# Optimization experiments

Hardware: AMD Instinct MI355X
Metric: run time of the kernel (lower is better)

Reference implementation:

```python
import jax, jax.numpy as jnp
import numpy as np

E = 384      # dim_embd
H = 6        # n_heads
D = E // H   # head dim = 64
T_MAX = 256  # block_size
EPS = 1e-5


def setup_inputs() -> dict:
    key = jax.random.key(0)
    ks = jax.random.split(key, 12)
    B, T = 128, 256
    s_in = (1.0 / E) ** 0.5
    s_ff = (1.0 / (4 * E)) ** 0.5
    return {
        "x": jax.random.normal(ks[0], (B, T, E), jnp.float32),
        # per-head projections stacked to match torch concat order: [E, H*D]
        "wq": jax.random.normal(ks[1], (E, E), jnp.float32) * s_in,
        "wk": jax.random.normal(ks[2], (E, E), jnp.float32) * s_in,
        "wv": jax.random.normal(ks[3], (E, E), jnp.float32) * s_in,
        "w_proj": jax.random.normal(ks[4], (E, E), jnp.float32) * s_in,
        "b_proj": jnp.zeros((E,), jnp.float32),
        "w1": jax.random.normal(ks[5], (E, 4 * E), jnp.float32) * s_in,
        "b1": jnp.zeros((4 * E,), jnp.float32),
        "w2": jax.random.normal(ks[6], (4 * E, E), jnp.float32) * s_ff,
        "b2": jnp.zeros((E,), jnp.float32),
        "g1": jnp.ones((E,), jnp.float32),
        "beta1": jnp.zeros((E,), jnp.float32),
        "g2": jnp.ones((E,), jnp.float32),
        "beta2": jnp.zeros((E,), jnp.float32),
    }


def _layernorm(x, g, b):
    mu = jnp.mean(x, axis=-1, keepdims=True)
    var = jnp.mean(jnp.square(x - mu), axis=-1, keepdims=True)
    return (x - mu) * jax.lax.rsqrt(var + EPS) * g + b


def _attention(x, wq, wk, wv, w_proj, b_proj):
    B, T, C = x.shape
    # batched per-head projections: [B,T,H,D]
    q = (x @ wq).reshape(B, T, H, D)
    k = (x @ wk).reshape(B, T, H, D)
    v = (x @ wv).reshape(B, T, H, D)
    # NOTE: original scales by C**-0.5 with C = full embed dim (384)
    scale = C ** (-0.5)
    scores = jnp.einsum("bthd,bshd->bhts", q, k) * scale
    mask = jnp.tril(jnp.ones((T, T), bool))
    scores = jnp.where(mask, scores, -jnp.inf)
    wei = jax.nn.softmax(scores, axis=-1)  # dropout = identity (eval)
    out = jnp.einsum("bhts,bshd->bthd", wei, v).reshape(B, T, C)
    return out @ w_proj + b_proj


def reference(x, wq, wk, wv, w_proj, b_proj, w1, b1, w2, b2, g1, beta1, g2, beta2):
    x = x + _attention(_layernorm(x, g1, beta1), wq, wk, wv, w_proj, b_proj)
    h = _layernorm(x, g2, beta2)
    h = jax.nn.relu(h @ w1 + b1) @ w2 + b2  # dropout = identity (eval)
    return x + h
```

## Files before the change

### kernel.cpp

```cpp
#include <hip/hip_runtime.h>
#include <hip/hip_bf16.h>

typedef __attribute__((ext_vector_type(8))) short bf16x8;
typedef __attribute__((ext_vector_type(4))) float f32x4;

#define MFMA_BF16(a, b, c) __builtin_amdgcn_mfma_f32_16x16x32_bf16((a), (b), (c), 0, 0, 0)

#define E_DIM 384
#define T_SEQ 256
#define B_BATCH 128
#define H_HEADS 6
#define D_HEAD 64
#define NROWS (B_BATCH * T_SEQ)
#define FF_DIM (4 * E_DIM)
#define QKV_LD 1152

__device__ __forceinline__ void load_lds16(const __hip_bfloat16* g, __hip_bfloat16* l) {
    __builtin_amdgcn_global_load_lds(
        (const __attribute__((address_space(1))) void*)g,
        (__attribute__((address_space(3))) void*)l, 16, 0, 0);
}

__device__ __forceinline__ float to_f(float x) { return x; }
__device__ __forceinline__ float to_f(__hip_bfloat16 x) { return __bfloat162float(x); }

__global__ void tcast_all_kernel(const float* __restrict__ wq, const float* __restrict__ wk,
                                 const float* __restrict__ wv, const float* __restrict__ wp,
                                 const float* __restrict__ w1, const float* __restrict__ w2,
                                 __hip_bfloat16* __restrict__ wqkvT, __hip_bfloat16* __restrict__ wpT,
                                 __hip_bfloat16* __restrict__ w1T, __hip_bfloat16* __restrict__ w2T) {
    const int WE = E_DIM * E_DIM;
    const int FE = E_DIM * FF_DIM;
    int idx = blockIdx.x * 256 + threadIdx.x;
    if (idx < 3 * WE) {
        int seg = idx / WE, j = idx - seg * WE;
        const float* W = seg == 0 ? wq : (seg == 1 ? wk : wv);
        int k = j / E_DIM, n = j - k * E_DIM;
        wqkvT[(size_t)seg * WE + (size_t)n * E_DIM + k] = __float2bfloat16(W[j]);
    } else if (idx < 4 * WE) {
        int j = idx - 3 * WE;
        int k = j / E_DIM, n = j - k * E_DIM;
        wpT[(size_t)n * E_DIM + k] = __float2bfloat16(wp[j]);
    } else if (idx < 4 * WE + FE) {
        int j = idx - 4 * WE;
        int k = j / FF_DIM, n = j - k * FF_DIM;
        w1T[(size_t)n * E_DIM + k] = __float2bfloat16(w1[j]);
    } else {
        int j = idx - 4 * WE - FE;
        int k = j / E_DIM, n = j - k * E_DIM;
        w2T[(size_t)n * FF_DIM + k] = __float2bfloat16(w2[j]);
    }
}

template <typename TI>
__global__ __launch_bounds__(256) void ln_kernel(const TI* __restrict__ x,
                                                 const float* __restrict__ g,
                                                 const float* __restrict__ bta,
                                                 __hip_bfloat16* __restrict__ out) {
    int row = blockIdx.x * 4 + (threadIdx.x >> 6);
    int lane = threadIdx.x & 63;
    const TI* xr = x + (size_t)row * E_DIM;
    float vals[6];
    float s = 0.f;
#pragma unroll
    for (int i = 0; i < 3; i++) {
        int c = i * 128 + 2 * lane;
        if constexpr (sizeof(TI) == 4) {
            float2 v = *reinterpret_cast<const float2*>(&xr[c]);
            vals[2 * i] = v.x;
            vals[2 * i + 1] = v.y;
        } else {
            ushort2 u = *reinterpret_cast<const ushort2*>(&xr[c]);
            union { unsigned short us; __hip_bfloat16 h; } a, b2;
            a.us = u.x; b2.us = u.y;
            vals[2 * i] = __bfloat162float(a.h);
            vals[2 * i + 1] = __bfloat162float(b2.h);
        }
        s += vals[2 * i] + vals[2 * i + 1];
    }
#pragma unroll
    for (int off = 1; off < 64; off <<= 1) s += __shfl_xor(s, off, 64);
    float mu = s * (1.f / E_DIM);
    float vv = 0.f;
#pragma unroll
    for (int i = 0; i < 6; i++) {
        float d = vals[i] - mu;
        vv += d * d;
    }
#pragma unroll
    for (int off = 1; off < 64; off <<= 1) vv += __shfl_xor(vv, off, 64);
    float rstd = rsqrtf(vv * (1.f / E_DIM) + 1e-5f);
#pragma unroll
    for (int i = 0; i < 3; i++) {
        int c = i * 128 + 2 * lane;
        float2 gv = *reinterpret_cast<const float2*>(&g[c]);
        float2 bv = *reinterpret_cast<const float2*>(&bta[c]);
        union { ushort2 u; struct { __hip_bfloat16 a, b; } h; } o2;
        o2.h.a = __float2bfloat16((vals[2 * i] - mu) * rstd * gv.x + bv.x);
        o2.h.b = __float2bfloat16((vals[2 * i + 1] - mu) * rstd * gv.y + bv.y);
        *reinterpret_cast<ushort2*>(&out[(size_t)row * E_DIM + c]) = o2.u;
    }
}

template <int EPI, int NW>
__global__ __launch_bounds__(NW * 64, NW == 8 ? 4 : 3) void gemm_kernel(
    const __hip_bfloat16* __restrict__ A, const __hip_bfloat16* __restrict__ BT,
    const float* __restrict__ bias, const void* __restrict__ resid,
    void* __restrict__ outp, int M, int N, int K) {
    constexpr int BM = NW * 32;
    constexpr int T = NW * 64;
    constexpr int BUF = (BM + 128) * 32;
    __shared__ __hip_bfloat16 lds[3 * BUF];
    const int t = threadIdx.x;
    const int w = t >> 6, lane = t & 63;
    const int l16 = lane & 15, lhi = lane >> 4;
    const int wm = w >> 1, wn = w & 1;

    const int nwg = gridDim.x;
    const int bid = blockIdx.x;
    const int cpx = nwg >> 3;
    const int swz = (bid & 7) * cpx + (bid >> 3);
    const int nb = N >> 7;
    const int m0 = (swz / nb) * BM;
    const int n0 = (swz % nb) * 128;

    const int ql = (t & 7) ^ ((t >> 3) & 7);
    const int sr = 2 * (t >> 3) + (ql >> 2);
    const int scol = (ql & 3) * 8;
    const __hip_bfloat16* pa0 = A + (size_t)(m0 + sr) * K + scol;
    const __hip_bfloat16* pa1 = pa0 + (size_t)(T / 4) * K;
    const __hip_bfloat16* pb0 = BT + (size_t)(n0 + sr) * K + scol;
    const __hip_bfloat16* pb1 = pb0 + (size_t)(T / 4) * K;
    const int dstA = t * 8;

    int aoff[4], boff[4];
#pragma unroll
    for (int mr = 0; mr < 4; mr++) {
        int R = wm * 64 + mr * 16 + l16;
        int L = R >> 1;
        int q = (((R & 1) << 2) | lhi) ^ (L & 7);
        aoff[mr] = L * 64 + q * 8;
    }
#pragma unroll
    for (int nr = 0; nr < 4; nr++) {
        int R = wn * 64 + nr * 16 + l16;
        int L = R >> 1;
        int q = (((R & 1) << 2) | lhi) ^ (L & 7);
        boff[nr] = BM * 32 + L * 64 + q * 8;
    }

    f32x4 acc[4][4] = {};
    const int nk = K >> 5;

#define STAGE(sbuf)                                                           \
    {                                                                         \
        __hip_bfloat16* sb_ = &lds[(sbuf) * BUF];                             \
        load_lds16(pa0, sb_ + dstA);                                          \
        load_lds16(pa1, sb_ + T * 8 + dstA);                                  \
        load_lds16(pb0, sb_ + BM * 32 + dstA);                                \
        if constexpr (NW == 4) load_lds16(pb1, sb_ + BM * 32 + T * 8 + dstA); \
        pa0 += 32;                                                            \
        pa1 += 32;                                                            \
        pb0 += 32;                                                            \
        if constexpr (NW == 4) pb1 += 32;                                     \
    }

    STAGE(0);
    STAGE(1);
    int rb = 0, sbx = 2;

    for (int kt = 0; kt < nk; kt++) {
        if (kt + 1 < nk) {
            if constexpr (NW == 8) asm volatile("s_waitcnt vmcnt(3)" ::: "memory");
            else                   asm volatile("s_waitcnt vmcnt(4)" ::: "memory");
        } else {
            asm volatile("s_waitcnt vmcnt(0)" ::: "memory");
        }
        __builtin_amdgcn_s_barrier();
        __builtin_amdgcn_sched_barrier(0);
        if (kt + 2 < nk) STAGE(sbx);
        const __hip_bfloat16* base = &lds[rb * BUF];
        bf16x8 af[4], bg[4];
#pragma unroll
        for (int mr = 0; mr < 4; mr++)
            af[mr] = *reinterpret_cast<const bf16x8*>(base + aoff[mr]);
#pragma unroll
        for (int nr = 0; nr < 4; nr++)
            bg[nr] = *reinterpret_cast<const bf16x8*>(base + boff[nr]);
        __builtin_amdgcn_s_setprio(1);
#pragma unroll
        for (int mr = 0; mr < 4; mr++)
#pragma unroll
            for (int nr = 0; nr < 4; nr++)
                acc[mr][nr] = MFMA_BF16(af[mr], bg[nr], acc[mr][nr]);
        __builtin_amdgcn_s_setprio(0);
        rb = rb == 2 ? 0 : rb + 1;
        sbx = sbx == 2 ? 0 : sbx + 1;
    }
#undef STAGE

    __hip_bfloat16* outb = (__hip_bfloat16*)outp;
    float* outf = (float*)outp;
#pragma unroll
    for (int mr = 0; mr < 4; mr++) {
#pragma unroll
        for (int nr = 0; nr < 4; nr++) {
            const int col = n0 + wn * 64 + nr * 16 + l16;
#pragma unroll
            for (int r = 0; r < 4; r++) {
                const int row = m0 + wm * 64 + mr * 16 + lhi * 4 + r;
                const size_t off = (size_t)row * N + col;
                float v = acc[mr][nr][r];
                if (EPI == 0) {
                    outb[off] = __float2bfloat16(v);
                } else if (EPI == 2) {
                    v += bias[col];
                    outb[off] = __float2bfloat16(v > 0.f ? v : 0.f);
                } else if (EPI == 3) {
                    v += bias[col] + ((const float*)resid)[off];
                    outb[off] = __float2bfloat16(v);
                } else {
                    v += bias[col] + to_f(((const __hip_bfloat16*)resid)[off]);
                    outf[off] = v;
                }
            }
        }
    }
}

__global__ __launch_bounds__(256, 2) void attn_kernel(
    const __hip_bfloat16* __restrict__ qkv, __hip_bfloat16* __restrict__ o) {
    __shared__ __hip_bfloat16 Ks[T_SEQ * 64];
    __shared__ __hip_bfloat16 VTs[64 * 256];
    __shared__ __hip_bfloat16 Ps[4 * 2048];

    const int bh = blockIdx.x;
    const int b = bh / H_HEADS, h = bh - b * H_HEADS;
    const int t = threadIdx.x;
    const int w = t >> 6, lane = t & 63;
    const int l16 = lane & 15, lhi = lane >> 4;
    const int l8 = l16 & 7;
    const size_t rbase = (size_t)b * T_SEQ;
    const int qoff = h * D_HEAD, koff = E_DIM + h * D_HEAD, voff = 2 * E_DIM + h * D_HEAD;
    const float qscale = 0.051031036307982884f * 1.4426950408889634f;

#pragma unroll
    for (int i = 0; i < 8; i++) {
        int idx = i * 256 + t;
        int r = idx >> 3;
        int c8 = idx & 7;
        load_lds16(qkv + (rbase + r) * QKV_LD + koff + ((c8 ^ (r & 7)) << 3),
                   &Ks[idx * 8]);
    }
#pragma unroll
    for (int i = 0; i < 8; i++) {
        int idx = i * 256 + t;
        int r = idx >> 3, d0 = (idx & 7) * 8;
        uint4 val = *reinterpret_cast<const uint4*>(qkv + (rbase + r) * QKV_LD + voff + d0);
        const __hip_bfloat16* p8 = reinterpret_cast<const __hip_bfloat16*>(&val);
        int slot = r >> 3, rin = r & 7;
#pragma unroll
        for (int j = 0; j < 8; j++) {
            int d = d0 + j;
            VTs[d * 256 + ((slot ^ (d & 7)) << 3) + rin] = p8[j];
        }
    }
    __syncthreads();

#pragma unroll
    for (int cp = 0; cp < 2; cp++) {
        const int c = cp ? 7 - w : w;
        bf16x8 qf[2][2];
#pragma unroll
        for (int mr = 0; mr < 2; mr++)
#pragma unroll
            for (int kk = 0; kk < 2; kk++)
                qf[mr][kk] = *reinterpret_cast<const bf16x8*>(
                    qkv + (rbase + c * 32 + mr * 16 + l16) * QKV_LD + qoff + kk * 32 + lhi * 8);

        float mstate[2][4], lstate[2][4];
        f32x4 oacc[2][4] = {};
#pragma unroll
        for (int mr = 0; mr < 2; mr++)
#pragma unroll
            for (int r = 0; r < 4; r++) {
                mstate[mr][r] = -1e30f;
                lstate[mr][r] = 0.f;
            }

        const int njt = (c >> 1) + 1;
        for (int jt = 0; jt < njt; jt++) {
            const bool diag = (jt == (c >> 1));
            f32x4 s[2][4] = {};
#pragma unroll
            for (int kk = 0; kk < 2; kk++) {
                bf16x8 kf[4];
#pragma unroll
                for (int nr = 0; nr < 4; nr++) {
                    int R = jt * 64 + nr * 16 + l16;
                    kf[nr] = *reinterpret_cast<const bf16x8*>(
                        &Ks[R * 64 + (((kk << 2) + lhi) ^ l8) * 8]);
                }
#pragma unroll
                for (int mr = 0; mr < 2; mr++)
#pragma unroll
                    for (int nr = 0; nr < 4; nr++)
                        s[mr][nr] = MFMA_BF16(qf[mr][kk], kf[nr], s[mr][nr]);
            }
#pragma unroll
            for (int mr = 0; mr < 2; mr++) {
#pragma unroll
                for (int r = 0; r < 4; r++) {
                    int qrow = c * 32 + mr * 16 + lhi * 4 + r;
                    float pv[4];
                    float mx = -1e30f;
                    if (diag) {
#pragma unroll
                        for (int nr = 0; nr < 4; nr++) {
                            int kcol = jt * 64 + nr * 16 + l16;
                            float val = s[mr][nr][r] * qscale;
                            if (kcol > qrow) val = -1e30f;
                            pv[nr] = val;
                            mx = fmaxf(mx, val);
                        }
                    } else {
#pragma unroll
                        for (int nr = 0; nr < 4; nr++) {
                            float val = s[mr][nr][r] * qscale;
                            pv[nr] = val;
                            mx = fmaxf(mx, val);
                        }
                    }
#pragma unroll
                    for (int off = 1; off < 16; off <<= 1)
                        mx = fmaxf(mx, __shfl_xor(mx, off, 64));
                    float mold = mstate[mr][r];
                    float mnew = fmaxf(mold, mx);
                    float corr = exp2f(mold - mnew);
                    float psum = 0.f;
#pragma unroll
                    for (int nr = 0; nr < 4; nr++) {
                        float p = exp2f(pv[nr] - mnew);
                        pv[nr] = p;
                        psum += p;
                    }
#pragma unroll
                    for (int off = 1; off < 16; off <<= 1)
                        psum += __shfl_xor(psum, off, 64);
                    lstate[mr][r] = lstate[mr][r] * corr + psum;
                    mstate[mr][r] = mnew;
#pragma unroll
                    for (int dr = 0; dr < 4; dr++) oacc[mr][dr][r] *= corr;
                    int pr = mr * 16 + lhi * 4 + r;
#pragma unroll
                    for (int nr = 0; nr < 4; nr++) {
                        int slot = (nr << 1) + (l16 >> 3);
                        Ps[w * 2048 + pr * 64 + ((slot ^ (pr & 7)) << 3) + l8] =
                            __float2bfloat16(pv[nr]);
                    }
                }
            }
#pragma unroll
            for (int kk = 0; kk < 2; kk++) {
                bf16x8 pa[2], vbf[4];
#pragma unroll
                for (int mr = 0; mr < 2; mr++) {
                    int row = mr * 16 + l16;
                    pa[mr] = *reinterpret_cast<const bf16x8*>(
                        &Ps[w * 2048 + row * 64 + (((kk << 2) + lhi) ^ l8) * 8]);
                }
#pragma unroll
                for (int dr = 0; dr < 4; dr++) {
                    int d = dr * 16 + l16;
                    int slot = (jt << 3) + (kk << 2) + lhi;
                    vbf[dr] = *reinterpret_cast<const bf16x8*>(
                        &VTs[d * 256 + ((slot ^ l8) << 3)]);
                }
#pragma unroll
                for (int mr = 0; mr < 2; mr++)
#pragma unroll
                    for (int dr = 0; dr < 4; dr++)
                        oacc[mr][dr] = MFMA_BF16(pa[mr], vbf[dr], oacc[mr][dr]);
            }
        }

#pragma unroll
        for (int mr = 0; mr < 2; mr++) {
#pragma unroll
            for (int r = 0; r < 4; r++) {
                float rl = 1.f / lstate[mr][r];
                int row = c * 32 + mr * 16 + lhi * 4 + r;
#pragma unroll
                for (int dr = 0; dr < 4; dr++)
                    o[(rbase + row) * E_DIM + h * D_HEAD + dr * 16 + l16] =
                        __float2bfloat16(oacc[mr][dr][r] * rl);
            }
        }
    }
}

extern "C" void kernel_launch(void* const* d_in, const int* in_sizes, int n_in,
                              void* d_out, int out_size, void* d_ws, size_t ws_size,
                              hipStream_t stream) {
    const float* x      = (const float*)d_in[0];
    const float* wq     = (const float*)d_in[1];
    const float* wk     = (const float*)d_in[2];
    const float* wv     = (const float*)d_in[3];
    const float* w_proj = (const float*)d_in[4];
    const float* b_proj = (const float*)d_in[5];
    const float* w1     = (const float*)d_in[6];
    const float* b1     = (const float*)d_in[7];
    const float* w2     = (const float*)d_in[8];
    const float* b2     = (const float*)d_in[9];
    const float* g1     = (const float*)d_in[10];
    const float* bt1    = (const float*)d_in[11];
    const float* g2     = (const float*)d_in[12];
    const float* bt2    = (const float*)d_in[13];
    float* out = (float*)d_out;

    char* ws = (char*)d_ws;
    size_t off = 0;
    auto alloc = [&](size_t bytes) {
        void* p = ws + off;
        off += (bytes + 255) & ~(size_t)255;
        return p;
    };
    const size_t wElems = E_DIM * E_DIM;
    const size_t fElems = E_DIM * FF_DIM;
    const size_t actElems = (size_t)NROWS * E_DIM;
    __hip_bfloat16* wqkvT = (__hip_bfloat16*)alloc(3 * wElems * 2);
    __hip_bfloat16* wpT   = (__hip_bfloat16*)alloc(wElems * 2);
    __hip_bfloat16* w1T   = (__hip_bfloat16*)alloc(fElems * 2);
    __hip_bfloat16* w2T   = (__hip_bfloat16*)alloc(fElems * 2);
    __hip_bfloat16* lnb   = (__hip_bfloat16*)alloc(actElems * 2);
    __hip_bfloat16* x2b   = (__hip_bfloat16*)alloc(actElems * 2);
    __hip_bfloat16* qkv   = (__hip_bfloat16*)alloc(3 * actElems * 2);
    __hip_bfloat16* ab    = (__hip_bfloat16*)alloc(actElems * 2);
    __hip_bfloat16* h1    = qkv;

    tcast_all_kernel<<<6912, 256, 0, stream>>>(wq, wk, wv, w_proj, w1, w2,
                                               wqkvT, wpT, w1T, w2T);

    ln_kernel<float><<<NROWS / 4, 256, 0, stream>>>(x, g1, bt1, lnb);

    gemm_kernel<0, 4><<<(NROWS / 128) * (QKV_LD / 128), 256, 0, stream>>>(
        lnb, wqkvT, nullptr, nullptr, qkv, NROWS, QKV_LD, E_DIM);

    attn_kernel<<<B_BATCH * H_HEADS, 256, 0, stream>>>(qkv, ab);

    gemm_kernel<3, 4><<<(NROWS / 128) * (E_DIM / 128), 256, 0, stream>>>(
        ab, wpT, b_proj, x, x2b, NROWS, E_DIM, E_DIM);

    ln_kernel<__hip_bfloat16><<<NROWS / 4, 256, 0, stream>>>(x2b, g2, bt2, lnb);

    gemm_kernel<2, 8><<<(NROWS / 256) * (FF_DIM / 128), 512, 0, stream>>>(
        lnb, w1T, b1, nullptr, h1, NROWS, FF_DIM, E_DIM);

    gemm_kernel<4, 4><<<(NROWS / 128) * (E_DIM / 128), 256, 0, stream>>>(
        h1, w2T, b2, x2b, out, NROWS, E_DIM, FF_DIM);
}
```

Baseline: 248.7 us.

## Add K=384 GEMM kernel keeping full B panel in LDS, A read directly

Adds a GEMM kernel for K=384 that loads an entire 64x384 panel of the transposed weight into swizzled LDS once. Each of 8 waves then streams its 64 rows of A straight from global memory into registers and runs MFMA. This replaces the pipelined LDS double-tiled GEMM for the QKV, output-projection and FF1 GEMMs. The aim is to drop the per-K-step A staging and barriers, at the cost of uncoalesced A loads with no reuse through LDS and A being re-read once per column block.

```diff
diff --git a/kernel.cpp b/kernel.cpp
--- a/kernel.cpp
+++ b/kernel.cpp
@@ -102,6 +102,101 @@
     }
 }
 
+template <int EPI>
+__global__ __launch_bounds__(512) void breg_gemm_kernel(
+    const __hip_bfloat16* __restrict__ A, const __hip_bfloat16* __restrict__ BT,
+    const float* __restrict__ bias, const float* __restrict__ resid,
+    void* __restrict__ outp, int M, int N) {
+    __shared__ __hip_bfloat16 Bs[64 * 384];
+    const int t = threadIdx.x;
+    const int w = t >> 6, lane = t & 63;
+    const int l16 = lane & 15, lhi = lane >> 4;
+
+    const int nwg = gridDim.x;
+    const int bid = blockIdx.x;
+    const int cpx = nwg >> 3;
+    const int swz = (bid & 7) * cpx + (bid >> 3);
+    const int nb = N >> 6;
+    const int m0 = (swz / nb) * 512;
+    const int n0 = (swz % nb) * 64;
+
+#pragma unroll
+    for (int c = 0; c < 6; c++) {
+        int u = c * 512 + t;
+        int r = u / 48;
+        int qp = u - r * 48;
+        int q = (qp & ~7) | ((qp & 7) ^ (r & 7));
+        load_lds16(BT + (size_t)(n0 + r) * 384 + q * 8, &Bs[u * 8]);
+    }
+
+    const __hip_bfloat16* pa[4][2];
+#pragma unroll
+    for (int mr = 0; mr < 4; mr++)
+#pragma unroll
+        for (int kk = 0; kk < 2; kk++)
+            pa[mr][kk] = A + (size_t)(m0 + w * 64 + mr * 16 + l16) * 384 + kk * 32 + lhi * 8;
+
+    int boff[4][2];
+#pragma unroll
+    for (int nr = 0; nr < 4; nr++)
+#pragma unroll
+        for (int kk = 0; kk < 2; kk++) {
+            int r = nr * 16 + l16;
+            boff[nr][kk] = r * 384 + (((kk * 4 + lhi) ^ (r & 7)) << 3);
+        }
+
+    __syncthreads();
+
+    f32x4 acc[4][4] = {};
+#pragma unroll
+    for (int kc = 0; kc < 6; kc++) {
+        bf16x8 af[4][2], bf_[4][2];
+#pragma unroll
+        for (int mr = 0; mr < 4; mr++)
+#pragma unroll
+            for (int kk = 0; kk < 2; kk++) {
+                af[mr][kk] = *reinterpret_cast<const bf16x8*>(pa[mr][kk]);
+                pa[mr][kk] += 64;
+            }
+#pragma unroll
+        for (int nr = 0; nr < 4; nr++)
+#pragma unroll
+            for (int kk = 0; kk < 2; kk++)
+                bf_[nr][kk] = *reinterpret_cast<const bf16x8*>(&Bs[boff[nr][kk] + kc * 64]);
+#pragma unroll
+        for (int kk = 0; kk < 2; kk++)
+#pragma unroll
+            for (int mr = 0; mr < 4; mr++)
+#pragma unroll
+                for (int nr = 0; nr < 4; nr++)
+                    acc[mr][nr] = MFMA_BF16(af[mr][kk], bf_[nr][kk], acc[mr][nr]);
+    }
+
+    __hip_bfloat16* outb = (__hip_bfloat16*)outp;
+#pragma unroll
+    for (int mr = 0; mr < 4; mr++) {
+#pragma unroll
+        for (int nr = 0; nr < 4; nr++) {
+            const int col = n0 + nr * 16 + l16;
+#pragma unroll
+            for (int r = 0; r < 4; r++) {
+                const int row = m0 + w * 64 + mr * 16 + lhi * 4 + r;
+                const size_t off = (size_t)row * N + col;
+                float v = acc[mr][nr][r];
+                if (EPI == 0) {
+                    outb[off] = __float2bfloat16(v);
+                } else if (EPI == 2) {
+                    v += bias[col];
+                    outb[off] = __float2bfloat16(v > 0.f ? v : 0.f);
+                } else {
+                    v += bias[col] + resid[off];
+                    outb[off] = __float2bfloat16(v);
+                }
+            }
+        }
+    }
+}
+
 template <int EPI, int NW>
 __global__ __launch_bounds__(NW * 64, NW == 8 ? 4 : 3) void gemm_kernel(
     const __hip_bfloat16* __restrict__ A, const __hip_bfloat16* __restrict__ BT,
@@ -443,18 +538,18 @@
 
     ln_kernel<float><<<NROWS / 4, 256, 0, stream>>>(x, g1, bt1, lnb);
 
-    gemm_kernel<0, 4><<<(NROWS / 128) * (QKV_LD / 128), 256, 0, stream>>>(
-        lnb, wqkvT, nullptr, nullptr, qkv, NROWS, QKV_LD, E_DIM);
+    breg_gemm_kernel<0><<<(NROWS / 512) * (QKV_LD / 64), 512, 0, stream>>>(
+        lnb, wqkvT, nullptr, nullptr, qkv, NROWS, QKV_LD);
 
     attn_kernel<<<B_BATCH * H_HEADS, 256, 0, stream>>>(qkv, ab);
 
-    gemm_kernel<3, 4><<<(NROWS / 128) * (E_DIM / 128), 256, 0, stream>>>(
-        ab, wpT, b_proj, x, x2b, NROWS, E_DIM, E_DIM);
+    breg_gemm_kernel<3><<<(NROWS / 512) * (E_DIM / 64), 512, 0, stream>>>(
+        ab, wpT, b_proj, x, x2b, NROWS, E_DIM);
 
     ln_kernel<__hip_bfloat16><<<NROWS / 4, 256, 0, stream>>>(x2b, g2, bt2, lnb);
 
-    gemm_kernel<2, 8><<<(NROWS / 256) * (FF_DIM / 128), 512, 0, stream>>>(
-        lnb, w1T, b1, nullptr, h1, NROWS, FF_DIM, E_DIM);
+    breg_gemm_kernel<2><<<(NROWS / 512) * (FF_DIM / 64), 512, 0, stream>>>(
+        lnb, w1T, b1, nullptr, h1, NROWS, FF_DIM);
 
     gemm_kernel<4, 4><<<(NROWS / 128) * (E_DIM / 128), 256, 0, stream>>>(
         h1, w2T, b2, x2b, out, NROWS, E_DIM, FF_DIM);
```

Result: slower. 338.5 us (+36.1%).

## Transpose score MFMA so softmax reductions stay in-lane, enlarge QKV GEMM tile

Applied to the files above, without the earlier changes.

The S=QK^T MFMA now takes its operands in swapped order, so each lane holds one query row's scores across several key columns. The row max and sum then need only two cross-lane shuffles per row block instead of four per register row. Softmax state shrinks to one value per lane, and the correction and normalisation factors are fetched into the output layout with __shfl. Separately, the QKV projection GEMM switches to the 256-row, 512-thread tile variant. The risks are the scattered bf16 stores into the P tile in LDS and extra shuffles for the correction broadcast.

```diff
diff --git a/kernel.cpp b/kernel.cpp
--- a/kernel.cpp
+++ b/kernel.cpp
@@ -278,15 +278,9 @@
                 qf[mr][kk] = *reinterpret_cast<const bf16x8*>(
                     qkv + (rbase + c * 32 + mr * 16 + l16) * QKV_LD + qoff + kk * 32 + lhi * 8);
 
-        float mstate[2][4], lstate[2][4];
+        float mstate[2] = {-1e30f, -1e30f};
+        float lstate[2] = {0.f, 0.f};
         f32x4 oacc[2][4] = {};
-#pragma unroll
-        for (int mr = 0; mr < 2; mr++)
-#pragma unroll
-            for (int r = 0; r < 4; r++) {
-                mstate[mr][r] = -1e30f;
-                lstate[mr][r] = 0.f;
-            }
 
         const int njt = (c >> 1) + 1;
         for (int jt = 0; jt < njt; jt++) {
@@ -305,60 +299,56 @@
                 for (int mr = 0; mr < 2; mr++)
 #pragma unroll
                     for (int nr = 0; nr < 4; nr++)
-                        s[mr][nr] = MFMA_BF16(qf[mr][kk], kf[nr], s[mr][nr]);
+                        s[mr][nr] = MFMA_BF16(kf[nr], qf[mr][kk], s[mr][nr]);
             }
 #pragma unroll
             for (int mr = 0; mr < 2; mr++) {
-#pragma unroll
-                for (int r = 0; r < 4; r++) {
-                    int qrow = c * 32 + mr * 16 + lhi * 4 + r;
-                    float pv[4];
-                    float mx = -1e30f;
-                    if (diag) {
-#pragma unroll
-                        for (int nr = 0; nr < 4; nr++) {
-                            int kcol = jt * 64 + nr * 16 + l16;
-                            float val = s[mr][nr][r] * qscale;
-                            if (kcol > qrow) val = -1e30f;
-                            pv[nr] = val;
-                            mx = fmaxf(mx, val);
-                        }
-                    } else {
-#pragma unroll
-                        for (int nr = 0; nr < 4; nr++) {
-                            float val = s[mr][nr][r] * qscale;
-                            pv[nr] = val;
-                            mx = fmaxf(mx, val);
-                        }
+                const int qrow = c * 32 + mr * 16 + l16;
+                float pv[4][4];
+                float mx = -1e30f;
+#pragma unroll
+                for (int nr = 0; nr < 4; nr++)
+#pragma unroll
+                    for (int r = 0; r < 4; r++) {
+                        int kcol = jt * 64 + nr * 16 + lhi * 4 + r;
+                        float val = s[mr][nr][r] * qscale;
+                        if (diag && kcol > qrow) val = -1e30f;
+                        pv[nr][r] = val;
+                        mx = fmaxf(mx, val);
                     }
-#pragma unroll
-                    for (int off = 1; off < 16; off <<= 1)
-                        mx = fmaxf(mx, __shfl_xor(mx, off, 64));
-                    float mold = mstate[mr][r];
-                    float mnew = fmaxf(mold, mx);
-                    float corr = exp2f(mold - mnew);
-                    float psum = 0.f;
-#pragma unroll
-                    for (int nr = 0; nr < 4; nr++) {
-                        float p = exp2f(pv[nr] - mnew);
-                        pv[nr] = p;
+                mx = fmaxf(mx, __shfl_xor(mx, 16, 64));
+                mx = fmaxf(mx, __shfl_xor(mx, 32, 64));
+                float mold = mstate[mr];
+                float mnew = fmaxf(mold, mx);
+                float corr = exp2f(mold - mnew);
+                float psum = 0.f;
+#pragma unroll
+                for (int nr = 0; nr < 4; nr++)
+#pragma unroll
+                    for (int r = 0; r < 4; r++) {
+                        float p = exp2f(pv[nr][r] - mnew);
+                        pv[nr][r] = p;
                         psum += p;
                     }
-#pragma unroll
-                    for (int off = 1; off < 16; off <<= 1)
-                        psum += __shfl_xor(psum, off, 64);
-                    lstate[mr][r] = lstate[mr][r] * corr + psum;
-                    mstate[mr][r] = mnew;
-#pragma unroll
-                    for (int dr = 0; dr < 4; dr++) oacc[mr][dr][r] *= corr;
-                    int pr = mr * 16 + lhi * 4 + r;
-#pragma unroll
-                    for (int nr = 0; nr < 4; nr++) {
-                        int slot = (nr << 1) + (l16 >> 3);
-                        Ps[w * 2048 + pr * 64 + ((slot ^ (pr & 7)) << 3) + l8] =
-                            __float2bfloat16(pv[nr]);
+                psum += __shfl_xor(psum, 16, 64);
+                psum += __shfl_xor(psum, 32, 64);
+                lstate[mr] = lstate[mr] * corr + psum;
+                mstate[mr] = mnew;
+#pragma unroll
+                for (int r = 0; r < 4; r++) {
+                    float cT = __shfl(corr, lhi * 4 + r, 64);
+#pragma unroll
+                    for (int dr = 0; dr < 4; dr++) oacc[mr][dr][r] *= cT;
+                }
+#pragma unroll
+                for (int nr = 0; nr < 4; nr++)
+#pragma unroll
+                    for (int r = 0; r < 4; r++) {
+                        int q = mr * 16 + l16;
+                        int kc = nr * 16 + lhi * 4 + r;
+                        Ps[w * 2048 + q * 64 + (((kc >> 3) ^ (q & 7)) << 3) + (kc & 7)] =
+                            __float2bfloat16(pv[nr][r]);
                     }
-                }
             }
 #pragma unroll
             for (int kk = 0; kk < 2; kk++) {
@@ -386,14 +376,15 @@
 
 #pragma unroll
         for (int mr = 0; mr < 2; mr++) {
+            float rl = 1.f / lstate[mr];
 #pragma unroll
             for (int r = 0; r < 4; r++) {
-                float rl = 1.f / lstate[mr][r];
+                float rlT = __shfl(rl, lhi * 4 + r, 64);
                 int row = c * 32 + mr * 16 + lhi * 4 + r;
 #pragma unroll
                 for (int dr = 0; dr < 4; dr++)
                     o[(rbase + row) * E_DIM + h * D_HEAD + dr * 16 + l16] =
-                        __float2bfloat16(oacc[mr][dr][r] * rl);
+                        __float2bfloat16(oacc[mr][dr][r] * rlT);
             }
         }
     }
@@ -443,7 +434,7 @@
 
     ln_kernel<float><<<NROWS / 4, 256, 0, stream>>>(x, g1, bt1, lnb);
 
-    gemm_kernel<0, 4><<<(NROWS / 128) * (QKV_LD / 128), 256, 0, stream>>>(
+    gemm_kernel<0, 8><<<(NROWS / 256) * (QKV_LD / 128), 512, 0, stream>>>(
         lnb, wqkvT, nullptr, nullptr, qkv, NROWS, QKV_LD, E_DIM);
 
     attn_kernel<<<B_BATCH * H_HEADS, 256, 0, stream>>>(qkv, ab);
```

Result: faster. 232.8 us (median of 2 runs) (-6.4%).
